# Kernel tuning notes

Measured on AMD Instinct MI355X. Metric: run time of the kernel, lower is better.

## Reference

```python
import jax, jax.numpy as jnp
import numpy as np

DEPTH, HEADS, DIM_HEAD, DIM = 4, 8, 64, 512
B, N = 4, 512
SCALE = DIM_HEAD ** -0.5  # attention scale
EPS = 1e-5


def _ln(r, g, b):
    # naive real-valued LayerNorm over last dim
    m = jnp.mean(r, -1, keepdims=True)
    v = jnp.mean((r - m) ** 2, -1, keepdims=True)
    return (r - m) / jnp.sqrt(v + EPS) * g + b


def _cln(z, gr, br, gi, bi):
    # 'layer_norm_naive': LN applied separately to real and imag parts
    return jax.lax.complex(_ln(jnp.real(z), gr, br), _ln(jnp.imag(z), gi, bi))


def _csoftmax(z):
    # softmax on magnitude, phase preserved (Eq. 36, arXiv:1802.08026)
    p = jax.nn.softmax(jnp.abs(z), axis=-1)
    ph = jnp.angle(z)
    return jax.lax.complex(p * jnp.cos(ph), p * jnp.sin(ph))


def _crelu(z):
    return jax.lax.complex(jax.nn.relu(jnp.real(z)), jax.nn.relu(jnp.imag(z)))


def setup_inputs():
    key = jax.random.key(0)
    ks = jax.random.split(key, 8)
    s = np.float32(1.0 / np.sqrt(DIM))
    return dict(
        x_real=jax.random.normal(ks[0], (B, N, DIM), jnp.float32),
        x_imag=jax.random.normal(ks[1], (B, N, DIM), jnp.float32),
        ln1_g_r=jnp.ones((DEPTH, DIM), jnp.float32),
        ln1_b_r=jnp.zeros((DEPTH, DIM), jnp.float32),
        ln1_g_i=jnp.ones((DEPTH, DIM), jnp.float32),
        ln1_b_i=jnp.zeros((DEPTH, DIM), jnp.float32),
        ln2_g_r=jnp.ones((DEPTH, DIM), jnp.float32),
        ln2_b_r=jnp.zeros((DEPTH, DIM), jnp.float32),
        ln2_g_i=jnp.ones((DEPTH, DIM), jnp.float32),
        ln2_b_i=jnp.zeros((DEPTH, DIM), jnp.float32),
        qkv_w_r=jax.random.normal(ks[2], (DEPTH, DIM, DIM), jnp.float32) * s,
        qkv_w_i=jax.random.normal(ks[3], (DEPTH, DIM, DIM), jnp.float32) * s,
        out_w_r=jax.random.normal(ks[4], (DEPTH, DIM, DIM), jnp.float32) * s,
        out_w_i=jax.random.normal(ks[5], (DEPTH, DIM, DIM), jnp.float32) * s,
        out_b_r=jnp.zeros((DEPTH, DIM), jnp.float32),
        out_b_i=jnp.zeros((DEPTH, DIM), jnp.float32),
        ff_w_r=jax.random.normal(ks[6], (DEPTH, DIM, DIM), jnp.float32) * s,
        ff_w_i=jax.random.normal(ks[7], (DEPTH, DIM, DIM), jnp.float32) * s,
        step_size=jnp.full((DEPTH,), 0.1, jnp.float32),
        lambd=jnp.full((DEPTH,), 0.1, jnp.float32),
    )


def reference(x_real, x_imag,
              ln1_g_r, ln1_b_r, ln1_g_i, ln1_b_i,
              ln2_g_r, ln2_b_r, ln2_g_i, ln2_b_i,
              qkv_w_r, qkv_w_i, out_w_r, out_w_i, out_b_r, out_b_i,
              ff_w_r, ff_w_i, step_size, lambd):
    x = jax.lax.complex(x_real, x_imag)  # [B, N, DIM] complex64
    for l in range(DEPTH):
        Wqkv = jax.lax.complex(qkv_w_r[l], qkv_w_i[l])  # [inner, dim]
        Wout = jax.lax.complex(out_w_r[l], out_w_i[l])  # [dim, inner]
        bout = jax.lax.complex(out_b_r[l], out_b_i[l])
        Wff = jax.lax.complex(ff_w_r[l], ff_w_i[l])     # [dim, dim]
        # --- PreNorm + Attention (single shared QKV projection) + residual
        xn = _cln(x, ln1_g_r[l], ln1_b_r[l], ln1_g_i[l], ln1_b_i[l])
        w = jnp.einsum('bnd,ed->bne', xn, Wqkv)                 # complex linear, no bias
        w = w.reshape(B, N, HEADS, DIM_HEAD).transpose(0, 2, 1, 3)  # b h n d
        dots = jnp.einsum('bhnd,bhmd->bhnm', w, jnp.conj(w)) * SCALE
        attn = _csoftmax(dots)
        out = jnp.einsum('bhnm,bhmd->bhnd', attn, w)
        out = out.transpose(0, 2, 1, 3).reshape(B, N, HEADS * DIM_HEAD)
        out = jnp.einsum('bne,de->bnd', out, Wout) + bout
        x = out + x
        # --- PreNorm + ISTA-style FeedForward (CReLU); no outer residual
        xn = _cln(x, ln2_g_r[l], ln2_b_r[l], ln2_g_i[l], ln2_b_i[l])
        ss = jax.nn.softplus(step_size[l])
        lm = jax.nn.softplus(lambd[l])
        x1 = jnp.einsum('bnd,ed->bne', xn, Wff)
        x = _crelu(xn + ss * x1 - ss * lm)
    # stack real/imag so the output is a plain float tensor [2, B, N, DIM]
    return jnp.stack([jnp.real(x), jnp.imag(x)], axis=0)
```

## Files before the change

### kernel.cpp

```cpp
#include <hip/hip_runtime.h>
#include <math.h>

#define DEPTHL 4
#define HEADS 8
#define DH 64
#define DIM 512
#define BATCH 4
#define SEQ 512
#define ROWS (BATCH*SEQ)
#define SCALE 0.125f
#define LNEPS 1e-5f

typedef __attribute__((ext_vector_type(8))) short bfrag;
typedef __attribute__((ext_vector_type(4))) float ffrag;
#define MFMA(a,b,c) __builtin_amdgcn_mfma_f32_16x16x32_bf16(a, b, c, 0, 0, 0)

__device__ __forceinline__ unsigned short f2bf(float f) {
    unsigned int u = __float_as_uint(f);
    u += 0x7fffu + ((u >> 16) & 1u);
    return (unsigned short)(u >> 16);
}
__device__ __forceinline__ float bf2f(unsigned short b) {
    return __uint_as_float(((unsigned int)b) << 16);
}

__global__ __launch_bounds__(256) void convw(
    const float* __restrict__ s0, const float* __restrict__ s1,
    const float* __restrict__ s2, const float* __restrict__ s3,
    const float* __restrict__ s4, const float* __restrict__ s5,
    unsigned short* __restrict__ dst)
{
    int gid = blockIdx.x * 256 + threadIdx.x;
    int idx = gid * 4;
    int seg = idx >> 18;
    int off = idx & 262143;
    const float* s = seg == 0 ? s0 : seg == 1 ? s1 : seg == 2 ? s2 :
                     seg == 3 ? s3 : seg == 4 ? s4 : s5;
    float4 v = *(const float4*)(s + off);
    unsigned long long p = (unsigned long long)f2bf(v.x)
        | ((unsigned long long)f2bf(v.y) << 16)
        | ((unsigned long long)f2bf(v.z) << 32)
        | ((unsigned long long)f2bf(v.w) << 48);
    *(unsigned long long*)(dst + idx) = p;
}

__device__ __forceinline__ void blk_sum4(float& a, float& b, float& c, float& d) {
    __shared__ float s[16];
    #pragma unroll
    for (int o = 32; o; o >>= 1) {
        a += __shfl_xor(a, o); b += __shfl_xor(b, o);
        c += __shfl_xor(c, o); d += __shfl_xor(d, o);
    }
    int w = threadIdx.x >> 6;
    if ((threadIdx.x & 63) == 0) { s[w*4+0]=a; s[w*4+1]=b; s[w*4+2]=c; s[w*4+3]=d; }
    __syncthreads();
    a = s[0]+s[4]+s[8]+s[12];
    b = s[1]+s[5]+s[9]+s[13];
    c = s[2]+s[6]+s[10]+s[14];
    d = s[3]+s[7]+s[11]+s[15];
    __syncthreads();
}

__global__ __launch_bounds__(256) void ln_kernel(
    const float* __restrict__ xr, const float* __restrict__ xi,
    const float* __restrict__ gr, const float* __restrict__ br,
    const float* __restrict__ gi, const float* __restrict__ bi,
    unsigned short* __restrict__ outr, unsigned short* __restrict__ outi)
{
    int row = blockIdx.x, t = threadIdx.x;
    float2 vr = ((const float2*)(xr + (size_t)row*DIM))[t];
    float2 vi = ((const float2*)(xi + (size_t)row*DIM))[t];
    float sr = vr.x+vr.y, qr = vr.x*vr.x+vr.y*vr.y;
    float si = vi.x+vi.y, qi = vi.x*vi.x+vi.y*vi.y;
    blk_sum4(sr, qr, si, qi);
    float mr = sr*(1.f/DIM), mi_ = si*(1.f/DIM);
    float rr = 1.f/sqrtf(qr*(1.f/DIM)-mr*mr+LNEPS);
    float ri = 1.f/sqrtf(qi*(1.f/DIM)-mi_*mi_+LNEPS);
    float2 g2r = ((const float2*)gr)[t], b2r = ((const float2*)br)[t];
    float2 g2i = ((const float2*)gi)[t], b2i = ((const float2*)bi)[t];
    float o0 = (vr.x-mr)*rr*g2r.x + b2r.x;
    float o1 = (vr.y-mr)*rr*g2r.y + b2r.y;
    float o2 = (vi.x-mi_)*ri*g2i.x + b2i.x;
    float o3 = (vi.y-mi_)*ri*g2i.y + b2i.y;
    unsigned int pr = (unsigned int)f2bf(o0) | ((unsigned int)f2bf(o1) << 16);
    unsigned int pi = (unsigned int)f2bf(o2) | ((unsigned int)f2bf(o3) << 16);
    ((unsigned int*)(outr + (size_t)row*DIM))[t] = pr;
    ((unsigned int*)(outi + (size_t)row*DIM))[t] = pi;
}

template<int MODE>
__global__ __launch_bounds__(256) void cgemm_mfma(
    const unsigned short* __restrict__ Ar, const unsigned short* __restrict__ Ai,
    const unsigned short* __restrict__ Wr, const unsigned short* __restrict__ Wi,
    unsigned short* __restrict__ Obr, unsigned short* __restrict__ Obi,
    float* __restrict__ Ofr, float* __restrict__ Ofi,
    const float* __restrict__ biasR, const float* __restrict__ biasI,
    const float* __restrict__ stepp, const float* __restrict__ lamb, int layer)
{
    int tid = threadIdx.x;
    int lane = tid & 63;
    int w = tid >> 6, wr = w >> 1, wc = w & 1;
    int lrow = lane & 15, lg = lane >> 4;
    int bm = blockIdx.x, bn = blockIdx.y;

    const unsigned short* pA_r[2]; const unsigned short* pA_i[2];
    const unsigned short* pB_r[2]; const unsigned short* pB_i[2];
    #pragma unroll
    for (int t = 0; t < 2; ++t) {
        int arow = bm*64 + wr*32 + t*16 + lrow;
        int brow = bn*64 + wc*32 + t*16 + lrow;
        pA_r[t] = Ar + (size_t)arow*DIM + lg*8;
        pA_i[t] = Ai + (size_t)arow*DIM + lg*8;
        pB_r[t] = Wr + (size_t)brow*DIM + lg*8;
        pB_i[t] = Wi + (size_t)brow*DIM + lg*8;
    }
    ffrag acc1[2][2], acc2[2][2], acci[2][2];
    #pragma unroll
    for (int a = 0; a < 2; ++a)
    #pragma unroll
    for (int b = 0; b < 2; ++b) {
        acc1[a][b] = (ffrag){0.f,0.f,0.f,0.f};
        acc2[a][b] = (ffrag){0.f,0.f,0.f,0.f};
        acci[a][b] = (ffrag){0.f,0.f,0.f,0.f};
    }

    #pragma unroll 2
    for (int k0 = 0; k0 < DIM; k0 += 32) {
        bfrag a_r[2], a_i[2], b_r[2], b_i[2];
        #pragma unroll
        for (int t = 0; t < 2; ++t) {
            a_r[t] = *(const bfrag*)(pA_r[t] + k0);
            a_i[t] = *(const bfrag*)(pA_i[t] + k0);
            b_r[t] = *(const bfrag*)(pB_r[t] + k0);
            b_i[t] = *(const bfrag*)(pB_i[t] + k0);
        }
        #pragma unroll
        for (int mt = 0; mt < 2; ++mt)
        #pragma unroll
        for (int nt = 0; nt < 2; ++nt) {
            acc1[mt][nt] = MFMA(a_r[mt], b_r[nt], acc1[mt][nt]);
            acc2[mt][nt] = MFMA(a_i[mt], b_i[nt], acc2[mt][nt]);
            acci[mt][nt] = MFMA(a_r[mt], b_i[nt], acci[mt][nt]);
            acci[mt][nt] = MFMA(a_i[mt], b_r[nt], acci[mt][nt]);
        }
    }

    float ss = 0.f, sl = 0.f;
    if (MODE == 2) { ss = log1pf(expf(stepp[layer])); sl = ss * log1pf(expf(lamb[layer])); }

    #pragma unroll
    for (int mt = 0; mt < 2; ++mt)
    #pragma unroll
    for (int nt = 0; nt < 2; ++nt) {
        int E = bn*64 + wc*32 + nt*16 + lrow;
        #pragma unroll
        for (int r = 0; r < 4; ++r) {
            int R = bm*64 + wr*32 + mt*16 + lg*4 + r;
            float re = acc1[mt][nt][r] - acc2[mt][nt][r];
            float im = acci[mt][nt][r];
            if (MODE == 0) {
                int b = R >> 9, n = R & (SEQ-1);
                int h = E >> 6, d = E & 63;
                size_t off = (((size_t)(b*HEADS + h)*SEQ + n) << 6) + d;
                Obr[off] = f2bf(re);
                Obi[off] = f2bf(im);
            } else if (MODE == 1) {
                size_t off = (size_t)R*DIM + E;
                Ofr[off] = re + biasR[E] + Ofr[off];
                Ofi[off] = im + biasI[E] + Ofi[off];
            } else {
                size_t off = (size_t)R*DIM + E;
                float xnr_ = bf2f(Ar[off]), xni_ = bf2f(Ai[off]);
                Ofr[off] = fmaxf(xnr_ + ss*re - sl, 0.f);
                Ofi[off] = fmaxf(xni_ + ss*im, 0.f);
            }
        }
    }
}

__global__ __launch_bounds__(256) void attn_mfma(
    const unsigned short* __restrict__ whr, const unsigned short* __restrict__ whi,
    unsigned short* __restrict__ aor, unsigned short* __restrict__ aoi)
{
    __shared__ unsigned short sVr[64][40], sVi[64][40];
    __shared__ unsigned short sPr[4][16][40], sPi[4][16][40];
    __shared__ unsigned short sO[64][72];
    int tid = threadIdx.x, lane = tid & 63, w = tid >> 6;
    int lrow = lane & 15, lg = lane >> 4;
    int bh = blockIdx.x, qt = blockIdx.y;
    const unsigned short* baseR = whr + ((size_t)bh << 15);
    const unsigned short* baseI = whi + ((size_t)bh << 15);
    int q0 = qt*64 + w*16;

    bfrag qfr[2], qfi[2];
    #pragma unroll
    for (int ks = 0; ks < 2; ++ks) {
        qfr[ks] = *(const bfrag*)(baseR + ((size_t)(q0 + lrow) << 6) + ks*32 + lg*8);
        qfi[ks] = *(const bfrag*)(baseI + ((size_t)(q0 + lrow) << 6) + ks*32 + lg*8);
    }
    float M = -1e30f, S = 0.f;
    ffrag o1[4], o2[4], o3[4];
    #pragma unroll
    for (int dt = 0; dt < 4; ++dt) {
        o1[dt] = (ffrag){0.f,0.f,0.f,0.f};
        o2[dt] = (ffrag){0.f,0.f,0.f,0.f};
        o3[dt] = (ffrag){0.f,0.f,0.f,0.f};
    }
    int sm = tid & 31;
    int sd = (tid >> 5) * 8;

    #pragma unroll 1
    for (int m0 = 0; m0 < SEQ; m0 += 32) {
        __syncthreads();
        {
            bfrag vr = *(const bfrag*)(baseR + ((size_t)(m0 + sm) << 6) + sd);
            bfrag vi = *(const bfrag*)(baseI + ((size_t)(m0 + sm) << 6) + sd);
            #pragma unroll
            for (int j = 0; j < 8; ++j) {
                sVr[sd + j][sm] = (unsigned short)vr[j];
                sVi[sd + j][sm] = (unsigned short)vi[j];
            }
        }
        ffrag zr[2], zp[2], zm_[2];
        #pragma unroll
        for (int t = 0; t < 2; ++t) {
            zr[t] = (ffrag){0.f,0.f,0.f,0.f};
            zp[t] = (ffrag){0.f,0.f,0.f,0.f};
            zm_[t] = (ffrag){0.f,0.f,0.f,0.f};
        }
        #pragma unroll
        for (int t = 0; t < 2; ++t)
        #pragma unroll
        for (int ks = 0; ks < 2; ++ks) {
            bfrag kr = *(const bfrag*)(baseR + ((size_t)(m0 + t*16 + lrow) << 6) + ks*32 + lg*8);
            bfrag ki = *(const bfrag*)(baseI + ((size_t)(m0 + t*16 + lrow) << 6) + ks*32 + lg*8);
            zr[t]  = MFMA(kr, qfr[ks], zr[t]);
            zr[t]  = MFMA(ki, qfi[ks], zr[t]);
            zp[t]  = MFMA(kr, qfi[ks], zp[t]);
            zm_[t] = MFMA(ki, qfr[ks], zm_[t]);
        }
        float av[2][4], rv[2][4], iv[2][4];
        float pmax = -1e30f;
        #pragma unroll
        for (int t = 0; t < 2; ++t)
        #pragma unroll
        for (int r = 0; r < 4; ++r) {
            float zrv = zr[t][r] * SCALE;
            float ziv = (zp[t][r] - zm_[t][r]) * SCALE;
            float a = sqrtf(zrv*zrv + ziv*ziv);
            av[t][r] = a; rv[t][r] = zrv; iv[t][r] = ziv;
            pmax = fmaxf(pmax, a);
        }
        pmax = fmaxf(pmax, __shfl_xor(pmax, 16));
        pmax = fmaxf(pmax, __shfl_xor(pmax, 32));
        float Mnew = fmaxf(M, pmax);
        float f = expf(M - Mnew);
        M = Mnew;
        S *= f;
        #pragma unroll
        for (int dt = 0; dt < 4; ++dt) { o1[dt] *= f; o2[dt] *= f; o3[dt] *= f; }
        float ssum = 0.f;
        #pragma unroll
        for (int t = 0; t < 2; ++t) {
            float ur[4], ui[4];
            #pragma unroll
            for (int r = 0; r < 4; ++r) {
                float a = av[t][r];
                float ee = expf(a - M);
                ssum += ee;
                float inva = a > 0.f ? ee / a : 0.f;
                ur[r] = a > 0.f ? inva * rv[t][r] : ee;
                ui[r] = inva * iv[t][r];
            }
            uint2 wpr, wpi;
            wpr.x = (unsigned int)f2bf(ur[0]) | ((unsigned int)f2bf(ur[1]) << 16);
            wpr.y = (unsigned int)f2bf(ur[2]) | ((unsigned int)f2bf(ur[3]) << 16);
            wpi.x = (unsigned int)f2bf(ui[0]) | ((unsigned int)f2bf(ui[1]) << 16);
            wpi.y = (unsigned int)f2bf(ui[2]) | ((unsigned int)f2bf(ui[3]) << 16);
            *(uint2*)&sPr[w][lrow][t*16 + lg*4] = wpr;
            *(uint2*)&sPi[w][lrow][t*16 + lg*4] = wpi;
        }
        ssum += __shfl_xor(ssum, 16);
        ssum += __shfl_xor(ssum, 32);
        S += ssum;
        __syncthreads();
        bfrag pr = *(const bfrag*)&sPr[w][lrow][lg*8];
        bfrag pi = *(const bfrag*)&sPi[w][lrow][lg*8];
        #pragma unroll
        for (int dt = 0; dt < 4; ++dt) {
            bfrag vr = *(const bfrag*)&sVr[dt*16 + lrow][lg*8];
            bfrag vi = *(const bfrag*)&sVi[dt*16 + lrow][lg*8];
            o1[dt] = MFMA(vr, pr, o1[dt]);
            o2[dt] = MFMA(vi, pi, o2[dt]);
            o3[dt] = MFMA(vr, pi, o3[dt]);
            o3[dt] = MFMA(vi, pr, o3[dt]);
        }
    }

    float invS = 1.f / S;
    int b = bh >> 3, h = bh & 7;
    __syncthreads();
    #pragma unroll
    for (int dt = 0; dt < 4; ++dt) {
        uint2 p;
        p.x = (unsigned int)f2bf((o1[dt][0]-o2[dt][0])*invS)
            | ((unsigned int)f2bf((o1[dt][1]-o2[dt][1])*invS) << 16);
        p.y = (unsigned int)f2bf((o1[dt][2]-o2[dt][2])*invS)
            | ((unsigned int)f2bf((o1[dt][3]-o2[dt][3])*invS) << 16);
        *(uint2*)&sO[w*16 + lrow][dt*16 + lg*4] = p;
    }
    __syncthreads();
    {
        int qrow = tid >> 2, d0 = (tid & 3) * 16;
        bfrag v0 = *(const bfrag*)&sO[qrow][d0];
        bfrag v1 = *(const bfrag*)&sO[qrow][d0 + 8];
        size_t off = (((size_t)(b*SEQ + qt*64 + qrow)) << 9) + h*64 + d0;
        *(bfrag*)(aor + off) = v0;
        *(bfrag*)(aor + off + 8) = v1;
    }
    __syncthreads();
    #pragma unroll
    for (int dt = 0; dt < 4; ++dt) {
        uint2 p;
        p.x = (unsigned int)f2bf(o3[dt][0]*invS) | ((unsigned int)f2bf(o3[dt][1]*invS) << 16);
        p.y = (unsigned int)f2bf(o3[dt][2]*invS) | ((unsigned int)f2bf(o3[dt][3]*invS) << 16);
        *(uint2*)&sO[w*16 + lrow][dt*16 + lg*4] = p;
    }
    __syncthreads();
    {
        int qrow = tid >> 2, d0 = (tid & 3) * 16;
        bfrag v0 = *(const bfrag*)&sO[qrow][d0];
        bfrag v1 = *(const bfrag*)&sO[qrow][d0 + 8];
        size_t off = (((size_t)(b*SEQ + qt*64 + qrow)) << 9) + h*64 + d0;
        *(bfrag*)(aoi + off) = v0;
        *(bfrag*)(aoi + off + 8) = v1;
    }
}

extern "C" void kernel_launch(void* const* d_in, const int* in_sizes, int n_in,
                              void* d_out, int out_size, void* d_ws, size_t ws_size,
                              hipStream_t stream)
{
    const float* x_real  = (const float*)d_in[0];
    const float* x_imag  = (const float*)d_in[1];
    const float* ln1_g_r = (const float*)d_in[2];
    const float* ln1_b_r = (const float*)d_in[3];
    const float* ln1_g_i = (const float*)d_in[4];
    const float* ln1_b_i = (const float*)d_in[5];
    const float* ln2_g_r = (const float*)d_in[6];
    const float* ln2_b_r = (const float*)d_in[7];
    const float* ln2_g_i = (const float*)d_in[8];
    const float* ln2_b_i = (const float*)d_in[9];
    const float* qkv_w_r = (const float*)d_in[10];
    const float* qkv_w_i = (const float*)d_in[11];
    const float* out_w_r = (const float*)d_in[12];
    const float* out_w_i = (const float*)d_in[13];
    const float* out_b_r = (const float*)d_in[14];
    const float* out_b_i = (const float*)d_in[15];
    const float* ff_w_r  = (const float*)d_in[16];
    const float* ff_w_i  = (const float*)d_in[17];
    const float* stepp   = (const float*)d_in[18];
    const float* lamb    = (const float*)d_in[19];

    const size_t SZ = (size_t)ROWS * DIM;
    const size_t WSEG = (size_t)DIM * DIM;
    float* xr = (float*)d_ws;
    float* xi = xr + SZ;
    unsigned short* xnr = (unsigned short*)(xi + SZ);
    unsigned short* xni = xnr + SZ;
    unsigned short* whr = xni + SZ;
    unsigned short* whi = whr + SZ;
    unsigned short* aor = whi + SZ;
    unsigned short* aoi = aor + SZ;
    unsigned short* wb  = aoi + SZ;

    hipMemcpyAsync(xr, x_real, SZ*sizeof(float), hipMemcpyDeviceToDevice, stream);
    hipMemcpyAsync(xi, x_imag, SZ*sizeof(float), hipMemcpyDeviceToDevice, stream);

    for (int l = 0; l < DEPTHL; ++l) {
        const size_t WO = (size_t)l * WSEG;
        convw<<<1536, 256, 0, stream>>>(qkv_w_r + WO, qkv_w_i + WO, out_w_r + WO,
                                        out_w_i + WO, ff_w_r + WO, ff_w_i + WO, wb);
        ln_kernel<<<ROWS, 256, 0, stream>>>(xr, xi,
            ln1_g_r + l*DIM, ln1_b_r + l*DIM, ln1_g_i + l*DIM, ln1_b_i + l*DIM, xnr, xni);
        cgemm_mfma<0><<<dim3(32, 8), 256, 0, stream>>>(xnr, xni, wb, wb + WSEG,
            whr, whi, nullptr, nullptr, nullptr, nullptr, nullptr, nullptr, l);
        attn_mfma<<<dim3(32, 8), 256, 0, stream>>>(whr, whi, aor, aoi);
        cgemm_mfma<1><<<dim3(32, 8), 256, 0, stream>>>(aor, aoi, wb + 2*WSEG, wb + 3*WSEG,
            nullptr, nullptr, xr, xi, out_b_r + l*DIM, out_b_i + l*DIM, nullptr, nullptr, l);
        ln_kernel<<<ROWS, 256, 0, stream>>>(xr, xi,
            ln2_g_r + l*DIM, ln2_b_r + l*DIM, ln2_g_i + l*DIM, ln2_b_i + l*DIM, xnr, xni);
        cgemm_mfma<2><<<dim3(32, 8), 256, 0, stream>>>(xnr, xni, wb + 4*WSEG, wb + 5*WSEG,
            nullptr, nullptr, xr, xi, nullptr, nullptr, stepp, lamb, l);
    }
    hipMemcpyAsync(d_out, xr, SZ*sizeof(float), hipMemcpyDeviceToDevice, stream);
    hipMemcpyAsync((float*)d_out + SZ, xi, SZ*sizeof(float), hipMemcpyDeviceToDevice, stream);
}
```

Before: 610.0 us.

## Split attention over key chunks per wave and halve GEMM row tiles

The attention kernel now gives each block only 16 queries and has its four waves process disjoint key ranges, each with private V/P shared buffers and no per-step block barriers. The per-wave softmax max and sum are merged through shared memory at the end. The complex GEMM moves to 32-row tiles with twice the grid and register prefetch of the next K slice, plus a launch-bounds occupancy hint. The last layer's feedforward writes straight into the output, which removes the final copies. These changes target low grid occupancy and barrier stalls, at the cost of reloading Q/K/V per block and a serialized cross-wave reduction.

```diff
diff --git a/kernel.cpp b/kernel.cpp
--- a/kernel.cpp
+++ b/kernel.cpp
@@ -89,7 +89,7 @@
 }
 
 template<int MODE>
-__global__ __launch_bounds__(256) void cgemm_mfma(
+__global__ __launch_bounds__(256, 4) void cgemm_mfma(
     const unsigned short* __restrict__ Ar, const unsigned short* __restrict__ Ai,
     const unsigned short* __restrict__ Wr, const unsigned short* __restrict__ Wi,
     unsigned short* __restrict__ Obr, unsigned short* __restrict__ Obi,
@@ -103,61 +103,67 @@
     int lrow = lane & 15, lg = lane >> 4;
     int bm = blockIdx.x, bn = blockIdx.y;
 
-    const unsigned short* pA_r[2]; const unsigned short* pA_i[2];
-    const unsigned short* pB_r[2]; const unsigned short* pB_i[2];
-    #pragma unroll
-    for (int t = 0; t < 2; ++t) {
-        int arow = bm*64 + wr*32 + t*16 + lrow;
-        int brow = bn*64 + wc*32 + t*16 + lrow;
-        pA_r[t] = Ar + (size_t)arow*DIM + lg*8;
-        pA_i[t] = Ai + (size_t)arow*DIM + lg*8;
-        pB_r[t] = Wr + (size_t)brow*DIM + lg*8;
-        pB_i[t] = Wi + (size_t)brow*DIM + lg*8;
-    }
-    ffrag acc1[2][2], acc2[2][2], acci[2][2];
-    #pragma unroll
-    for (int a = 0; a < 2; ++a)
-    #pragma unroll
-    for (int b = 0; b < 2; ++b) {
-        acc1[a][b] = (ffrag){0.f,0.f,0.f,0.f};
-        acc2[a][b] = (ffrag){0.f,0.f,0.f,0.f};
-        acci[a][b] = (ffrag){0.f,0.f,0.f,0.f};
-    }
+    const unsigned short* pAr = Ar + (size_t)(bm*32 + wr*16 + lrow)*DIM + lg*8;
+    const unsigned short* pAi = Ai + (size_t)(bm*32 + wr*16 + lrow)*DIM + lg*8;
+    const unsigned short* pBr[2]; const unsigned short* pBi[2];
+    #pragma unroll
+    for (int nt = 0; nt < 2; ++nt) {
+        int brow = bn*64 + wc*32 + nt*16 + lrow;
+        pBr[nt] = Wr + (size_t)brow*DIM + lg*8;
+        pBi[nt] = Wi + (size_t)brow*DIM + lg*8;
+    }
+    ffrag acc1[2], acc2[2], acci[2];
+    #pragma unroll
+    for (int nt = 0; nt < 2; ++nt) {
+        acc1[nt] = (ffrag){0.f,0.f,0.f,0.f};
+        acc2[nt] = (ffrag){0.f,0.f,0.f,0.f};
+        acci[nt] = (ffrag){0.f,0.f,0.f,0.f};
+    }
+
+    bfrag a_r = *(const bfrag*)(pAr);
+    bfrag a_i = *(const bfrag*)(pAi);
+    bfrag b_r0 = *(const bfrag*)(pBr[0]), b_r1 = *(const bfrag*)(pBr[1]);
+    bfrag b_i0 = *(const bfrag*)(pBi[0]), b_i1 = *(const bfrag*)(pBi[1]);
 
     #pragma unroll 2
-    for (int k0 = 0; k0 < DIM; k0 += 32) {
-        bfrag a_r[2], a_i[2], b_r[2], b_i[2];
-        #pragma unroll
-        for (int t = 0; t < 2; ++t) {
-            a_r[t] = *(const bfrag*)(pA_r[t] + k0);
-            a_i[t] = *(const bfrag*)(pA_i[t] + k0);
-            b_r[t] = *(const bfrag*)(pB_r[t] + k0);
-            b_i[t] = *(const bfrag*)(pB_i[t] + k0);
-        }
-        #pragma unroll
-        for (int mt = 0; mt < 2; ++mt)
-        #pragma unroll
-        for (int nt = 0; nt < 2; ++nt) {
-            acc1[mt][nt] = MFMA(a_r[mt], b_r[nt], acc1[mt][nt]);
-            acc2[mt][nt] = MFMA(a_i[mt], b_i[nt], acc2[mt][nt]);
-            acci[mt][nt] = MFMA(a_r[mt], b_i[nt], acci[mt][nt]);
-            acci[mt][nt] = MFMA(a_i[mt], b_r[nt], acci[mt][nt]);
-        }
-    }
+    for (int k0 = 0; k0 < DIM - 32; k0 += 32) {
+        bfrag na_r = *(const bfrag*)(pAr + k0 + 32);
+        bfrag na_i = *(const bfrag*)(pAi + k0 + 32);
+        bfrag nb_r0 = *(const bfrag*)(pBr[0] + k0 + 32);
+        bfrag nb_r1 = *(const bfrag*)(pBr[1] + k0 + 32);
+        bfrag nb_i0 = *(const bfrag*)(pBi[0] + k0 + 32);
+        bfrag nb_i1 = *(const bfrag*)(pBi[1] + k0 + 32);
+        acc1[0] = MFMA(a_r, b_r0, acc1[0]);
+        acc2[0] = MFMA(a_i, b_i0, acc2[0]);
+        acci[0] = MFMA(a_r, b_i0, acci[0]);
+        acci[0] = MFMA(a_i, b_r0, acci[0]);
+        acc1[1] = MFMA(a_r, b_r1, acc1[1]);
+        acc2[1] = MFMA(a_i, b_i1, acc2[1]);
+        acci[1] = MFMA(a_r, b_i1, acci[1]);
+        acci[1] = MFMA(a_i, b_r1, acci[1]);
+        a_r = na_r; a_i = na_i;
+        b_r0 = nb_r0; b_r1 = nb_r1; b_i0 = nb_i0; b_i1 = nb_i1;
+    }
+    acc1[0] = MFMA(a_r, b_r0, acc1[0]);
+    acc2[0] = MFMA(a_i, b_i0, acc2[0]);
+    acci[0] = MFMA(a_r, b_i0, acci[0]);
+    acci[0] = MFMA(a_i, b_r0, acci[0]);
+    acc1[1] = MFMA(a_r, b_r1, acc1[1]);
+    acc2[1] = MFMA(a_i, b_i1, acc2[1]);
+    acci[1] = MFMA(a_r, b_i1, acci[1]);
+    acci[1] = MFMA(a_i, b_r1, acci[1]);
 
     float ss = 0.f, sl = 0.f;
     if (MODE == 2) { ss = log1pf(expf(stepp[layer])); sl = ss * log1pf(expf(lamb[layer])); }
 
     #pragma unroll
-    for (int mt = 0; mt < 2; ++mt)
-    #pragma unroll
     for (int nt = 0; nt < 2; ++nt) {
         int E = bn*64 + wc*32 + nt*16 + lrow;
         #pragma unroll
         for (int r = 0; r < 4; ++r) {
-            int R = bm*64 + wr*32 + mt*16 + lg*4 + r;
-            float re = acc1[mt][nt][r] - acc2[mt][nt][r];
-            float im = acci[mt][nt][r];
+            int R = bm*32 + wr*16 + lg*4 + r;
+            float re = acc1[nt][r] - acc2[nt][r];
+            float im = acci[nt][r];
             if (MODE == 0) {
                 int b = R >> 9, n = R & (SEQ-1);
                 int h = E >> 6, d = E & 63;
@@ -178,19 +184,24 @@
     }
 }
 
-__global__ __launch_bounds__(256) void attn_mfma(
+#define SVI(w_, ri, d, m) ((((w_)*2 + (ri))*64 + (d))*40 + (m))
+#define SPI(w_, ri, q, m) (20480 + (((w_)*2 + (ri))*16 + (q))*40 + (m))
+
+__global__ __launch_bounds__(256, 3) void attn_mfma(
     const unsigned short* __restrict__ whr, const unsigned short* __restrict__ whi,
     unsigned short* __restrict__ aor, unsigned short* __restrict__ aoi)
 {
-    __shared__ unsigned short sVr[64][40], sVi[64][40];
-    __shared__ unsigned short sPr[4][16][40], sPi[4][16][40];
-    __shared__ unsigned short sO[64][72];
+    __shared__ __align__(16) unsigned short pool[25856];
+    float* sMS = (float*)(pool + 25600);
+    float* sAccR = (float*)pool;
+    float* sAccI = sAccR + 64*16;
+
     int tid = threadIdx.x, lane = tid & 63, w = tid >> 6;
     int lrow = lane & 15, lg = lane >> 4;
     int bh = blockIdx.x, qt = blockIdx.y;
     const unsigned short* baseR = whr + ((size_t)bh << 15);
     const unsigned short* baseI = whi + ((size_t)bh << 15);
-    int q0 = qt*64 + w*16;
+    int q0 = qt*16;
 
     bfrag qfr[2], qfi[2];
     #pragma unroll
@@ -206,19 +217,21 @@
         o2[dt] = (ffrag){0.f,0.f,0.f,0.f};
         o3[dt] = (ffrag){0.f,0.f,0.f,0.f};
     }
-    int sm = tid & 31;
-    int sd = (tid >> 5) * 8;
+    const int sm = lane & 31;
+    const int sdb = ((lane >> 5) & 1) * 8;
 
     #pragma unroll 1
-    for (int m0 = 0; m0 < SEQ; m0 += 32) {
-        __syncthreads();
-        {
-            bfrag vr = *(const bfrag*)(baseR + ((size_t)(m0 + sm) << 6) + sd);
-            bfrag vi = *(const bfrag*)(baseI + ((size_t)(m0 + sm) << 6) + sd);
+    for (int rd = 0; rd < 4; ++rd) {
+        int m0 = rd*128 + w*32;
+        #pragma unroll
+        for (int it = 0; it < 4; ++it) {
+            int d0 = sdb + it*16;
+            bfrag vr = *(const bfrag*)(baseR + ((size_t)(m0 + sm) << 6) + d0);
+            bfrag vi = *(const bfrag*)(baseI + ((size_t)(m0 + sm) << 6) + d0);
             #pragma unroll
             for (int j = 0; j < 8; ++j) {
-                sVr[sd + j][sm] = (unsigned short)vr[j];
-                sVi[sd + j][sm] = (unsigned short)vi[j];
+                pool[SVI(w, 0, d0 + j, sm)] = (unsigned short)vr[j];
+                pool[SVI(w, 1, d0 + j, sm)] = (unsigned short)vi[j];
             }
         }
         ffrag zr[2], zp[2], zm_[2];
@@ -277,19 +290,18 @@
             wpr.y = (unsigned int)f2bf(ur[2]) | ((unsigned int)f2bf(ur[3]) << 16);
             wpi.x = (unsigned int)f2bf(ui[0]) | ((unsigned int)f2bf(ui[1]) << 16);
             wpi.y = (unsigned int)f2bf(ui[2]) | ((unsigned int)f2bf(ui[3]) << 16);
-            *(uint2*)&sPr[w][lrow][t*16 + lg*4] = wpr;
-            *(uint2*)&sPi[w][lrow][t*16 + lg*4] = wpi;
+            *(uint2*)&pool[SPI(w, 0, lrow, t*16 + lg*4)] = wpr;
+            *(uint2*)&pool[SPI(w, 1, lrow, t*16 + lg*4)] = wpi;
         }
         ssum += __shfl_xor(ssum, 16);
         ssum += __shfl_xor(ssum, 32);
         S += ssum;
-        __syncthreads();
-        bfrag pr = *(const bfrag*)&sPr[w][lrow][lg*8];
-        bfrag pi = *(const bfrag*)&sPi[w][lrow][lg*8];
+        bfrag pr = *(const bfrag*)&pool[SPI(w, 0, lrow, lg*8)];
+        bfrag pi = *(const bfrag*)&pool[SPI(w, 1, lrow, lg*8)];
         #pragma unroll
         for (int dt = 0; dt < 4; ++dt) {
-            bfrag vr = *(const bfrag*)&sVr[dt*16 + lrow][lg*8];
-            bfrag vi = *(const bfrag*)&sVi[dt*16 + lrow][lg*8];
+            bfrag vr = *(const bfrag*)&pool[SVI(w, 0, dt*16 + lrow, lg*8)];
+            bfrag vi = *(const bfrag*)&pool[SVI(w, 1, dt*16 + lrow, lg*8)];
             o1[dt] = MFMA(vr, pr, o1[dt]);
             o2[dt] = MFMA(vi, pi, o2[dt]);
             o3[dt] = MFMA(vr, pi, o3[dt]);
@@ -297,43 +309,48 @@
         }
     }
 
-    float invS = 1.f / S;
-    int b = bh >> 3, h = bh & 7;
+    if (lg == 0) { sMS[(w*2 + 0)*16 + lrow] = M; sMS[(w*2 + 1)*16 + lrow] = S; }
     __syncthreads();
-    #pragma unroll
-    for (int dt = 0; dt < 4; ++dt) {
-        uint2 p;
-        p.x = (unsigned int)f2bf((o1[dt][0]-o2[dt][0])*invS)
-            | ((unsigned int)f2bf((o1[dt][1]-o2[dt][1])*invS) << 16);
-        p.y = (unsigned int)f2bf((o1[dt][2]-o2[dt][2])*invS)
-            | ((unsigned int)f2bf((o1[dt][3]-o2[dt][3])*invS) << 16);
-        *(uint2*)&sO[w*16 + lrow][dt*16 + lg*4] = p;
-    }
-    __syncthreads();
+    float Mf = -1e30f;
+    #pragma unroll
+    for (int w2 = 0; w2 < 4; ++w2) Mf = fmaxf(Mf, sMS[(w2*2 + 0)*16 + lrow]);
+    float Sf = 0.f;
+    #pragma unroll
+    for (int w2 = 0; w2 < 4; ++w2)
+        Sf += sMS[(w2*2 + 1)*16 + lrow] * expf(sMS[(w2*2 + 0)*16 + lrow] - Mf);
+    float fac = expf(M - Mf) / Sf;
+
+    #pragma unroll 1
+    for (int ww = 0; ww < 4; ++ww) {
+        if (w == ww) {
+            #pragma unroll
+            for (int dt = 0; dt < 4; ++dt)
+            #pragma unroll
+            for (int r = 0; r < 4; ++r) {
+                int d = dt*16 + lg*4 + r;
+                float vR = (o1[dt][r] - o2[dt][r]) * fac;
+                float vI = o3[dt][r] * fac;
+                if (ww == 0) { sAccR[d*16 + lrow] = vR; sAccI[d*16 + lrow] = vI; }
+                else         { sAccR[d*16 + lrow] += vR; sAccI[d*16 + lrow] += vI; }
+            }
+        }
+        __syncthreads();
+    }
     {
-        int qrow = tid >> 2, d0 = (tid & 3) * 16;
-        bfrag v0 = *(const bfrag*)&sO[qrow][d0];
-        bfrag v1 = *(const bfrag*)&sO[qrow][d0 + 8];
-        size_t off = (((size_t)(b*SEQ + qt*64 + qrow)) << 9) + h*64 + d0;
-        *(bfrag*)(aor + off) = v0;
-        *(bfrag*)(aor + off + 8) = v1;
-    }
-    __syncthreads();
-    #pragma unroll
-    for (int dt = 0; dt < 4; ++dt) {
-        uint2 p;
-        p.x = (unsigned int)f2bf(o3[dt][0]*invS) | ((unsigned int)f2bf(o3[dt][1]*invS) << 16);
-        p.y = (unsigned int)f2bf(o3[dt][2]*invS) | ((unsigned int)f2bf(o3[dt][3]*invS) << 16);
-        *(uint2*)&sO[w*16 + lrow][dt*16 + lg*4] = p;
-    }
-    __syncthreads();
-    {
-        int qrow = tid >> 2, d0 = (tid & 3) * 16;
-        bfrag v0 = *(const bfrag*)&sO[qrow][d0];
-        bfrag v1 = *(const bfrag*)&sO[qrow][d0 + 8];
-        size_t off = (((size_t)(b*SEQ + qt*64 + qrow)) << 9) + h*64 + d0;
-        *(bfrag*)(aoi + off) = v0;
-        *(bfrag*)(aoi + off + 8) = v1;
+        int q = tid >> 4, d0 = (tid & 15) * 4;
+        int b = bh >> 3, h = bh & 7;
+        float r0 = sAccR[(d0+0)*16 + q], r1 = sAccR[(d0+1)*16 + q];
+        float r2 = sAccR[(d0+2)*16 + q], r3 = sAccR[(d0+3)*16 + q];
+        float i0 = sAccI[(d0+0)*16 + q], i1 = sAccI[(d0+1)*16 + q];
+        float i2 = sAccI[(d0+2)*16 + q], i3 = sAccI[(d0+3)*16 + q];
+        uint2 pr, pi;
+        pr.x = (unsigned int)f2bf(r0) | ((unsigned int)f2bf(r1) << 16);
+        pr.y = (unsigned int)f2bf(r2) | ((unsigned int)f2bf(r3) << 16);
+        pi.x = (unsigned int)f2bf(i0) | ((unsigned int)f2bf(i1) << 16);
+        pi.y = (unsigned int)f2bf(i2) | ((unsigned int)f2bf(i3) << 16);
+        size_t off = (((size_t)(bh >> 3)*SEQ + qt*16 + q) << 9) + (bh & 7)*64 + d0;
+        *(uint2*)(aor + off) = pr;
+        *(uint2*)(aoi + off) = pi;
     }
 }
 
@@ -374,6 +391,9 @@
     unsigned short* aoi = aor + SZ;
     unsigned short* wb  = aoi + SZ;
 
+    float* outR = (float*)d_out;
+    float* outI = outR + SZ;
+
     hipMemcpyAsync(xr, x_real, SZ*sizeof(float), hipMemcpyDeviceToDevice, stream);
     hipMemcpyAsync(xi, x_imag, SZ*sizeof(float), hipMemcpyDeviceToDevice, stream);
 
@@ -383,16 +403,16 @@
                                         out_w_i + WO, ff_w_r + WO, ff_w_i + WO, wb);
         ln_kernel<<<ROWS, 256, 0, stream>>>(xr, xi,
             ln1_g_r + l*DIM, ln1_b_r + l*DIM, ln1_g_i + l*DIM, ln1_b_i + l*DIM, xnr, xni);
-        cgemm_mfma<0><<<dim3(32, 8), 256, 0, stream>>>(xnr, xni, wb, wb + WSEG,
+        cgemm_mfma<0><<<dim3(64, 8), 256, 0, stream>>>(xnr, xni, wb, wb + WSEG,
             whr, whi, nullptr, nullptr, nullptr, nullptr, nullptr, nullptr, l);
-        attn_mfma<<<dim3(32, 8), 256, 0, stream>>>(whr, whi, aor, aoi);
-        cgemm_mfma<1><<<dim3(32, 8), 256, 0, stream>>>(aor, aoi, wb + 2*WSEG, wb + 3*WSEG,
+        attn_mfma<<<dim3(32, 32), 256, 0, stream>>>(whr, whi, aor, aoi);
+        cgemm_mfma<1><<<dim3(64, 8), 256, 0, stream>>>(aor, aoi, wb + 2*WSEG, wb + 3*WSEG,
             nullptr, nullptr, xr, xi, out_b_r + l*DIM, out_b_i + l*DIM, nullptr, nullptr, l);
         ln_kernel<<<ROWS, 256, 0, stream>>>(xr, xi,
             ln2_g_r + l*DIM, ln2_b_r + l*DIM, ln2_g_i + l*DIM, ln2_b_i + l*DIM, xnr, xni);
-        cgemm_mfma<2><<<dim3(32, 8), 256, 0, stream>>>(xnr, xni, wb + 4*WSEG, wb + 5*WSEG,
-            nullptr, nullptr, xr, xi, nullptr, nullptr, stepp, lamb, l);
-    }
-    hipMemcpyAsync(d_out, xr, SZ*sizeof(float), hipMemcpyDeviceToDevice, stream);
-    hipMemcpyAsync((float*)d_out + SZ, xi, SZ*sizeof(float), hipMemcpyDeviceToDevice, stream);
-}
+        float* dstR = (l == DEPTHL-1) ? outR : xr;
+        float* dstI = (l == DEPTHL-1) ? outI : xi;
+        cgemm_mfma<2><<<dim3(64, 8), 256, 0, stream>>>(xnr, xni, wb + 4*WSEG, wb + 5*WSEG,
+            nullptr, nullptr, dstR, dstI, nullptr, nullptr, stepp, lamb, l);
+    }
+}
```

New measurement: 657.8 us. 7.8% more time.
